# Performance work log

Measured on AMD Instinct MI355X. Metric: run time of the kernel, lower is better.

## Reference

```python
import jax, jax.numpy as jnp
import numpy as np

LN_EPS = 1e-6

def _layernorm(x, g, b):
    mu = jnp.mean(x, axis=-1, keepdims=True)
    var = jnp.mean((x - mu) ** 2, axis=-1, keepdims=True)
    return (x - mu) / jnp.sqrt(var + LN_EPS) * g + b

def _mha(q, k, v, wq, bq, wk, bk, wv, bv, fc, fcb, ln_g, ln_b, n_head, d_k, d_v):
    # standard post-LN multi-head attention (residual + layernorm), eval mode (no dropout)
    b, lq, _ = q.shape
    bk_, lk, _ = k.shape
    residual = q
    qh = (q @ wq + bq).reshape(b, lq, n_head, d_k).transpose(0, 2, 1, 3)      # [b,h,lq,dk]
    kh = (k @ wk + bk).reshape(bk_, lk, n_head, d_k).transpose(0, 2, 1, 3)    # [bk,h,lk,dk]
    vh = (v @ wv + bv).reshape(bk_, lk, n_head, d_v).transpose(0, 2, 1, 3)    # [bk,h,lk,dv]
    attn = jax.nn.softmax(jnp.matmul(qh, kh.swapaxes(-1, -2)) / (d_k ** 0.5), axis=-1)  # [b,h,lq,lk]
    out = jnp.matmul(attn, vh)                                                # [b,h,lq,dv]
    out = out.transpose(0, 2, 1, 3).reshape(b, lq, n_head * d_v)
    pre = out
    out = _layernorm(out @ fc + fcb + residual, ln_g, ln_b)
    return out, attn, pre


def setup_inputs() -> dict:
    key = jax.random.key(0)
    ks = jax.random.split(key, 32)
    B, C, H, W = 16, 64, 32, 32
    NC, D = 5, 96  # num_classes, memory feature dim
    s = 0.05
    d = {
        'x': jax.random.normal(ks[0], (B, C, H, W), jnp.float32),
        'memory': jax.random.normal(ks[1], (NC, D), jnp.float32),
        'wb_w': jax.random.normal(ks[2], (C, NC), jnp.float32) * s,
        'wb_b': jnp.zeros((NC,), jnp.float32),
        # slf_attn: n_head=1, d_model=64, d_input_k=96, d_k=96, d_v=64
        'a1_wq': jax.random.normal(ks[3], (64, 96), jnp.float32) * s,
        'a1_bq': jnp.zeros((96,), jnp.float32),
        'a1_wk': jax.random.normal(ks[4], (96, 96), jnp.float32) * s,
        'a1_bk': jnp.zeros((96,), jnp.float32),
        'a1_wv': jax.random.normal(ks[5], (96, 64), jnp.float32) * s,
        'a1_bv': jnp.zeros((64,), jnp.float32),
        'a1_fc': jax.random.normal(ks[6], (64, 64), jnp.float32) * s,
        'a1_fcb': jnp.zeros((64,), jnp.float32),
        'a1_ln_g': jnp.ones((64,), jnp.float32),
        'a1_ln_b': jnp.zeros((64,), jnp.float32),
        # slf_attn1: n_head=4, d_model=64, d_input_k=64, d_k=64, d_v=64
        'a2_wq': jax.random.normal(ks[7], (64, 256), jnp.float32) * s,
        'a2_bq': jnp.zeros((256,), jnp.float32),
        'a2_wk': jax.random.normal(ks[8], (64, 256), jnp.float32) * s,
        'a2_bk': jnp.zeros((256,), jnp.float32),
        'a2_wv': jax.random.normal(ks[9], (64, 256), jnp.float32) * s,
        'a2_bv': jnp.zeros((256,), jnp.float32),
        'a2_fc': jax.random.normal(ks[10], (256, 64), jnp.float32) * s,
        'a2_fcb': jnp.zeros((64,), jnp.float32),
        'a2_ln_g': jnp.ones((64,), jnp.float32),
        'a2_ln_b': jnp.zeros((64,), jnp.float32),
    }
    return d


def reference(x, memory, wb_w, wb_b,
              a1_wq, a1_bq, a1_wk, a1_bk, a1_wv, a1_bv, a1_fc, a1_fcb, a1_ln_g, a1_ln_b,
              a2_wq, a2_bq, a2_wk, a2_bk, a2_wv, a2_bv, a2_fc, a2_fcb, a2_ln_g, a2_ln_b):
    b, c, H, W = x.shape
    xt = x.transpose(0, 2, 3, 1).reshape(b, H * W, c)            # [b,HW,64]
    weight = xt @ wb_w + wb_b                                    # [b,HW,5]
    weight1 = jax.nn.softmax(weight, axis=-1)                    # softmax over classes
    weight2 = jax.nn.softmax(weight.transpose(0, 2, 1), axis=-1) # [b,5,HW], softmax over HW
    class_feat1 = jnp.matmul(weight2, xt)                        # [b,5,64] class-weighted pooling
    mem = memory[None]                                           # [1,5,96]
    cf, _, _ = _mha(class_feat1, mem, mem,
                    a1_wq, a1_bq, a1_wk, a1_bk, a1_wv, a1_bv, a1_fc, a1_fcb, a1_ln_g, a1_ln_b,
                    n_head=1, d_k=96, d_v=64)                    # [b,5,64]
    cf = jnp.matmul(weight1, cf)                                 # redistribution [b,HW,64]
    cf, _, _ = _mha(cf, cf, cf,
                    a2_wq, a2_bq, a2_wk, a2_bk, a2_wv, a2_bv, a2_fc, a2_fcb, a2_ln_g, a2_ln_b,
                    n_head=4, d_k=64, d_v=64)                    # [b,HW,64]
    return cf.transpose(0, 2, 1).reshape(-1, 64, H, W)           # [b,64,H,W]
```

## Files before the change

kernel.cpp:

```cpp
#include <hip/hip_runtime.h>
#include <math.h>

typedef unsigned short ushort_t;
typedef __attribute__((ext_vector_type(8))) short short8;
typedef __attribute__((ext_vector_type(4))) float f32x4;

#define B_  16
#define HW_ 1024
#define C_  64
#define NC_ 5
#define D1_ 96
#define NH_ 4
#define DH_ 64

#define MFMA32(A,B,C) __builtin_amdgcn_mfma_f32_16x16x32_bf16(A,B,C,0,0,0)

__device__ __forceinline__ ushort_t f2bf(float f) {
    unsigned u = __float_as_uint(f);
    u = u + 0x7fffu + ((u >> 16) & 1u);
    return (ushort_t)(u >> 16);
}

__device__ __forceinline__ unsigned pack2_trunc(float lo, float hi) {
    return (__float_as_uint(hi) & 0xffff0000u) | (__float_as_uint(lo) >> 16);
}
__device__ __forceinline__ unsigned pack2_rne(float lo, float hi) {
    return ((unsigned)f2bf(hi) << 16) | (unsigned)f2bf(lo);
}
__device__ __forceinline__ float bf_lo(unsigned u) { return __uint_as_float(u << 16); }
__device__ __forceinline__ float bf_hi(unsigned u) { return __uint_as_float(u & 0xffff0000u); }

__global__ __launch_bounds__(64) void k1_logits(const float* __restrict__ x,
                                                const float* __restrict__ wb_w,
                                                const float* __restrict__ wb_b,
                                                float* __restrict__ logitsT,
                                                float* __restrict__ w1) {
    int b = blockIdx.x >> 4;
    int hw = (blockIdx.x & 15) * 64 + threadIdx.x;
    const float* xb = x + (size_t)b * C_ * HW_;
    float acc[NC_];
#pragma unroll
    for (int j = 0; j < NC_; j++) acc[j] = wb_b[j];
#pragma unroll 8
    for (int c = 0; c < C_; c++) {
        float xv = xb[c * HW_ + hw];
#pragma unroll
        for (int j = 0; j < NC_; j++) acc[j] += xv * wb_w[c * NC_ + j];
    }
    float m = acc[0];
#pragma unroll
    for (int j = 1; j < NC_; j++) m = fmaxf(m, acc[j]);
    float e[NC_], s = 0.f;
#pragma unroll
    for (int j = 0; j < NC_; j++) { e[j] = __expf(acc[j] - m); s += e[j]; }
    float inv = 1.f / s;
    int idx = b * HW_ + hw;
#pragma unroll
    for (int j = 0; j < NC_; j++) {
        logitsT[((size_t)b * NC_ + j) * HW_ + hw] = acc[j];
        w1[(size_t)idx * NC_ + j] = e[j] * inv;
    }
}

__global__ __launch_bounds__(256) void k2b_pool(const float* __restrict__ x,
                                                const float* __restrict__ logitsT,
                                                float* __restrict__ cf1) {
    __shared__ float pl[NC_ * HW_];
    __shared__ float sinv[NC_];
    int t = threadIdx.x;
    int b = blockIdx.x >> 4, chg = blockIdx.x & 15;
    const float* lp = logitsT + (size_t)b * NC_ * HW_;
    for (int i = t * 4; i < NC_ * HW_; i += 1024)
        *(float4*)(pl + i) = *(const float4*)(lp + i);
    __syncthreads();
    int w = t >> 6, lane = t & 63;
    for (int r = w; r < NC_; r += 4) {
        float m = -1e30f;
        for (int i = lane; i < HW_; i += 64) m = fmaxf(m, pl[r * HW_ + i]);
#pragma unroll
        for (int off = 1; off < 64; off <<= 1) m = fmaxf(m, __shfl_xor(m, off, 64));
        float s = 0.f;
        for (int i = lane; i < HW_; i += 64) {
            float e = __expf(pl[r * HW_ + i] - m);
            pl[r * HW_ + i] = e;
            s += e;
        }
#pragma unroll
        for (int off = 1; off < 64; off <<= 1) s += __shfl_xor(s, off, 64);
        if (lane == 0) sinv[r] = 1.f / s;
    }
    __syncthreads();
    int ch = chg * 4 + w;
    const float* xc = x + ((size_t)b * C_ + ch) * HW_;
    float acc[NC_] = {0.f, 0.f, 0.f, 0.f, 0.f};
#pragma unroll
    for (int i = 0; i < HW_ / 64; i++) {
        int hw = i * 64 + lane;
        float xv = xc[hw];
#pragma unroll
        for (int c = 0; c < NC_; c++) acc[c] += xv * pl[c * HW_ + hw];
    }
#pragma unroll
    for (int c = 0; c < NC_; c++) {
        float a = acc[c];
#pragma unroll
        for (int off = 1; off < 64; off <<= 1) a += __shfl_xor(a, off, 64);
        if (lane == 0) cf1[((size_t)b * NC_ + c) * C_ + ch] = a * sinv[c];
    }
}

__global__ __launch_bounds__(256) void k3_mha1(const float* __restrict__ cf1,
                                               const float* __restrict__ wq, const float* __restrict__ bq,
                                               const float* __restrict__ mem,
                                               const float* __restrict__ wk, const float* __restrict__ bk,
                                               const float* __restrict__ wv, const float* __restrict__ bv,
                                               const float* __restrict__ fc, const float* __restrict__ fcb,
                                               const float* __restrict__ lng, const float* __restrict__ lnb,
                                               float* __restrict__ cfs) {
    __shared__ float cs[NC_ * C_];
    __shared__ float kh[NC_ * D1_];
    __shared__ float vh[NC_ * DH_];
    __shared__ float q[NC_ * D1_];
    __shared__ float sc[NC_ * NC_];
    __shared__ float pp[NC_ * NC_];
    __shared__ float o[NC_ * C_];
    __shared__ float z[NC_ * C_];
    __shared__ float mu[NC_], rs[NC_];
    int t = threadIdx.x, b = blockIdx.x;
    for (int i = t; i < NC_ * C_; i += 256) cs[i] = cf1[(size_t)b * NC_ * C_ + i];
    for (int idx = t; idx < NC_ * D1_; idx += 256) {
        int i = idx / D1_, k = idx % D1_;
        float a = bk[k];
        for (int d = 0; d < D1_; d++) a += mem[i * D1_ + d] * wk[d * D1_ + k];
        kh[idx] = a;
    }
    for (int idx = t; idx < NC_ * DH_; idx += 256) {
        int i = idx / DH_, dv = idx % DH_;
        float a = bv[dv];
        for (int d = 0; d < D1_; d++) a += mem[i * D1_ + d] * wv[d * DH_ + dv];
        vh[idx] = a;
    }
    __syncthreads();
    for (int idx = t; idx < NC_ * D1_; idx += 256) {
        int i = idx / D1_, k = idx % D1_;
        float a = bq[k];
        for (int c = 0; c < C_; c++) a += cs[i * C_ + c] * wq[c * D1_ + k];
        q[idx] = a;
    }
    __syncthreads();
    if (t < NC_ * NC_) {
        int i = t / NC_, j = t % NC_;
        float a = 0.f;
        for (int k = 0; k < D1_; k++) a += q[i * D1_ + k] * kh[j * D1_ + k];
        sc[t] = a * 0.1020620726159657f;
    }
    __syncthreads();
    if (t < NC_) {
        float m = sc[t * NC_];
        for (int j = 1; j < NC_; j++) m = fmaxf(m, sc[t * NC_ + j]);
        float e[NC_], s = 0.f;
        for (int j = 0; j < NC_; j++) { e[j] = __expf(sc[t * NC_ + j] - m); s += e[j]; }
        float inv = 1.f / s;
        for (int j = 0; j < NC_; j++) pp[t * NC_ + j] = e[j] * inv;
    }
    __syncthreads();
    for (int idx = t; idx < NC_ * C_; idx += 256) {
        int i = idx / C_, dv = idx % C_;
        float a = 0.f;
        for (int j = 0; j < NC_; j++) a += pp[i * NC_ + j] * vh[j * C_ + dv];
        o[idx] = a;
    }
    __syncthreads();
    for (int idx = t; idx < NC_ * C_; idx += 256) {
        int i = idx / C_, dd = idx % C_;
        float a = fcb[dd] + cs[idx];
        for (int c2 = 0; c2 < C_; c2++) a += o[i * C_ + c2] * fc[c2 * C_ + dd];
        z[idx] = a;
    }
    __syncthreads();
    if (t < NC_) {
        float s = 0.f;
        for (int d = 0; d < C_; d++) s += z[t * C_ + d];
        float mm = s / C_;
        float v = 0.f;
        for (int d = 0; d < C_; d++) { float dd2 = z[t * C_ + d] - mm; v += dd2 * dd2; }
        mu[t] = mm; rs[t] = rsqrtf(v / C_ + 1e-6f);
    }
    __syncthreads();
    for (int idx = t; idx < NC_ * C_; idx += 256) {
        int i = idx / C_, dd = idx % C_;
        cfs[(size_t)b * NC_ * C_ + idx] = (z[idx] - mu[i]) * rs[i] * lng[dd] + lnb[dd];
    }
}

__global__ __launch_bounds__(256) void k5_mfma(const float* __restrict__ w1,
                                               const float* __restrict__ cfs,
                                               const float* __restrict__ wq, const float* __restrict__ bq,
                                               const float* __restrict__ wk, const float* __restrict__ bk,
                                               const float* __restrict__ wv, const float* __restrict__ bv,
                                               ushort_t* __restrict__ Qb, ushort_t* __restrict__ Kb,
                                               ushort_t* __restrict__ Vt) {
    __shared__ ushort_t Af[64][68];
    __shared__ ushort_t Wt[256][68];
    int t = threadIdx.x;
    int which = blockIdx.y;
    int m0 = blockIdx.x * 64;
    int b = m0 >> 10, lbase = m0 & 1023;
    {
        int r = t >> 2, ks = (t & 3) * 16;
        const float* cp = cfs + (size_t)b * NC_ * C_;
        const float* w1p = w1 + (size_t)(m0 + r) * NC_;
        float v0 = w1p[0], v1 = w1p[1], v2 = w1p[2], v3 = w1p[3], v4 = w1p[4];
#pragma unroll
        for (int j = 0; j < 16; j += 2) {
            int k = ks + j;
            float e0 = v0 * cp[k]       + v1 * cp[64 + k]     + v2 * cp[128 + k]
                     + v3 * cp[192 + k] + v4 * cp[256 + k];
            float e1 = v0 * cp[k + 1]     + v1 * cp[64 + k + 1] + v2 * cp[128 + k + 1]
                     + v3 * cp[192 + k + 1] + v4 * cp[256 + k + 1];
            *(unsigned*)&Af[r][k] = pack2_rne(e0, e1);
        }
    }
    const float* W = (which == 0) ? wq : (which == 1) ? wk : wv;
    {
        int n = t;
#pragma unroll
        for (int k = 0; k < 64; k += 2) {
            *(unsigned*)&Wt[n][k] = pack2_rne(W[k * 256 + n], W[(k + 1) * 256 + n]);
        }
    }
    __syncthreads();
    int lane = t & 63, w = t >> 6;
    int l15 = lane & 15, quad = lane >> 4;
    if (which < 2) {
        const float* bias = (which == 0) ? bq : bk;
        float scale = (which == 0) ? 0.18033688011112042f : 1.0f;
        ushort_t* dst = (which == 0) ? Qb : Kb;
        short8 a0[4], a1[4];
#pragma unroll
        for (int mi = 0; mi < 4; mi++) {
            a0[mi] = *(const short8*)&Af[mi * 16 + l15][quad * 8];
            a1[mi] = *(const short8*)&Af[mi * 16 + l15][32 + quad * 8];
        }
#pragma unroll
        for (int nt = 0; nt < 4; nt++) {
            int ni = w * 4 + nt;
            short8 b0 = *(const short8*)&Wt[ni * 16 + l15][quad * 8];
            short8 b1 = *(const short8*)&Wt[ni * 16 + l15][32 + quad * 8];
            int n = ni * 16 + l15;
            float bb = bias[n];
            int h = n >> 6, dd = n & 63;
#pragma unroll
            for (int mi = 0; mi < 4; mi++) {
                f32x4 z = {0, 0, 0, 0};
                f32x4 dv4 = MFMA32(a0[mi], b0, z);
                dv4 = MFMA32(a1[mi], b1, dv4);
                size_t base = ((size_t)(b * NH_ + h) * HW_ + (lbase + mi * 16 + quad * 4)) * DH_ + dd;
#pragma unroll
                for (int r = 0; r < 4; r++)
                    dst[base + (size_t)r * DH_] = f2bf((dv4[r] + bb) * scale);
            }
        }
    } else {
        short8 a0[4], a1[4];
#pragma unroll
        for (int mt = 0; mt < 4; mt++) {
            int mi = w * 4 + mt;
            a0[mt] = *(const short8*)&Wt[mi * 16 + l15][quad * 8];
            a1[mt] = *(const short8*)&Wt[mi * 16 + l15][32 + quad * 8];
        }
#pragma unroll
        for (int nt = 0; nt < 4; nt++) {
            short8 b0 = *(const short8*)&Af[nt * 16 + l15][quad * 8];
            short8 b1 = *(const short8*)&Af[nt * 16 + l15][32 + quad * 8];
#pragma unroll
            for (int mt = 0; mt < 4; mt++) {
                int mi = w * 4 + mt;
                f32x4 z = {0, 0, 0, 0};
                f32x4 dv4 = MFMA32(a0[mt], b0, z);
                dv4 = MFMA32(a1[mt], b1, dv4);
                int h = mi >> 2;
#pragma unroll
                for (int r = 0; r < 4; r++) {
                    int nw = mi * 16 + quad * 4 + r;
                    int dv = nw & 63;
                    Vt[((size_t)(b * NH_ + h) * DH_ + dv) * HW_ + lbase + nt * 16 + l15] =
                        f2bf(dv4[r] + bv[nw]);
                }
            }
        }
    }
}

__global__ __launch_bounds__(256) void k6_attn(const ushort_t* __restrict__ Qb,
                                               const ushort_t* __restrict__ Kb,
                                               const ushort_t* __restrict__ Vt,
                                               ushort_t* __restrict__ aoP0, ushort_t* __restrict__ aoP1,
                                               float* __restrict__ sP0, float* __restrict__ sP1) {
    int t = threadIdx.x;
    int w = t >> 6;
    int lane = t & 63;
    int l15 = lane & 15;
    int quad = lane >> 4;
    int L = blockIdx.x;
    int bh = ((L >> 3) & 7) * 8 + (L & 7);
    int khalf = (L >> 6) & 1;
    int qt = L >> 7;
    int b = bh >> 2, h = bh & 3;
    const ushort_t* Qp = Qb + (size_t)bh * HW_ * DH_;
    const ushort_t* Kp = Kb + (size_t)bh * HW_ * DH_;
    const ushort_t* Vp = Vt + (size_t)bh * DH_ * HW_;
    int row0 = qt * 256 + w * 16;
    short8 q0[4], q1[4];
#pragma unroll
    for (int tl = 0; tl < 4; tl++) {
        const ushort_t* qp = Qp + (size_t)(row0 + tl * 64 + l15) * DH_ + quad * 8;
        q0[tl] = *(const short8*)(qp);
        q1[tl] = *(const short8*)(qp + 32);
    }
    int f0 = ((l15 >> 2) * 8) + (l15 & 3);
    int kstart = khalf * 512;
    const ushort_t* K0p = Kp + (size_t)(kstart + f0) * DH_ + quad * 8;
    const ushort_t* K1p = Kp + (size_t)(kstart + f0 + 4) * DH_ + quad * 8;
    const ushort_t* Vp0 = Vp + (size_t)(0 * 16 + l15) * HW_ + kstart + quad * 8;
    const ushort_t* Vp1 = Vp + (size_t)(1 * 16 + l15) * HW_ + kstart + quad * 8;
    const ushort_t* Vp2 = Vp + (size_t)(2 * 16 + l15) * HW_ + kstart + quad * 8;
    const ushort_t* Vp3 = Vp + (size_t)(3 * 16 + l15) * HW_ + kstart + quad * 8;
    const short ONE = (short)0x3F80;
    short8 ones = {ONE, ONE, ONE, ONE, ONE, ONE, ONE, ONE};
    f32x4 o0[4], o1[4], o2[4], o3[4], oS[4];
#pragma unroll
    for (int tl = 0; tl < 4; tl++) {
        o0[tl] = (f32x4){0,0,0,0}; o1[tl] = (f32x4){0,0,0,0};
        o2[tl] = (f32x4){0,0,0,0}; o3[tl] = (f32x4){0,0,0,0};
        oS[tl] = (f32x4){0,0,0,0};
    }
    for (int kt = 0; kt < 16; kt++) {
        int kbase = kt * 32;
        size_t koff = (size_t)kbase * DH_;
        short8 ka0 = *(const short8*)(K0p + koff);
        short8 ka1 = *(const short8*)(K0p + koff + 32);
        short8 kb0 = *(const short8*)(K1p + koff);
        short8 kb1 = *(const short8*)(K1p + koff + 32);
        short8 v0 = *(const short8*)(Vp0 + kbase);
        short8 v1 = *(const short8*)(Vp1 + kbase);
        short8 v2 = *(const short8*)(Vp2 + kbase);
        short8 v3 = *(const short8*)(Vp3 + kbase);
        f32x4 z = {0,0,0,0};
#pragma unroll
        for (int tl = 0; tl < 4; tl++) {
            f32x4 s0 = MFMA32(ka0, q0[tl], z);  s0 = MFMA32(ka1, q1[tl], s0);
            f32x4 s1 = MFMA32(kb0, q0[tl], z);  s1 = MFMA32(kb1, q1[tl], s1);
            float p0 = exp2f(s0[0]), p1 = exp2f(s0[1]), p2 = exp2f(s0[2]), p3 = exp2f(s0[3]);
            float p4 = exp2f(s1[0]), p5 = exp2f(s1[1]), p6 = exp2f(s1[2]), p7 = exp2f(s1[3]);
            union { short8 v; unsigned u[4]; } pf;
            pf.u[0] = pack2_trunc(p0, p1);  pf.u[1] = pack2_trunc(p2, p3);
            pf.u[2] = pack2_trunc(p4, p5);  pf.u[3] = pack2_trunc(p6, p7);
            o0[tl] = MFMA32(v0, pf.v, o0[tl]);
            o1[tl] = MFMA32(v1, pf.v, o1[tl]);
            o2[tl] = MFMA32(v2, pf.v, o2[tl]);
            o3[tl] = MFMA32(v3, pf.v, o3[tl]);
            oS[tl] = MFMA32(ones, pf.v, oS[tl]);
        }
    }
    ushort_t* aoP = khalf ? aoP1 : aoP0;
    float* sP = khalf ? sP1 : sP0;
#pragma unroll
    for (int tl = 0; tl < 4; tl++) {
        int rowg = row0 + tl * 64 + l15;
        ushort_t* aop = aoP + ((size_t)(b * HW_ + rowg)) * 256 + h * 64 + quad * 4;
        uint2 u;
        u.x = pack2_trunc(o0[tl][0], o0[tl][1]); u.y = pack2_trunc(o0[tl][2], o0[tl][3]);
        *(uint2*)(aop + 0) = u;
        u.x = pack2_trunc(o1[tl][0], o1[tl][1]); u.y = pack2_trunc(o1[tl][2], o1[tl][3]);
        *(uint2*)(aop + 16) = u;
        u.x = pack2_trunc(o2[tl][0], o2[tl][1]); u.y = pack2_trunc(o2[tl][2], o2[tl][3]);
        *(uint2*)(aop + 32) = u;
        u.x = pack2_trunc(o3[tl][0], o3[tl][1]); u.y = pack2_trunc(o3[tl][2], o3[tl][3]);
        *(uint2*)(aop + 48) = u;
        if (quad == 0)
            sP[(size_t)(b * HW_ + rowg) * NH_ + h] = oS[tl][0];
    }
}

__global__ __launch_bounds__(256) void k7_final(const ushort_t* __restrict__ aoP0,
                                                const ushort_t* __restrict__ aoP1,
                                                const float* __restrict__ sP0,
                                                const float* __restrict__ sP1,
                                                const float* __restrict__ w1,
                                                const float* __restrict__ cfs,
                                                const float* __restrict__ fc, const float* __restrict__ fcb,
                                                const float* __restrict__ lng, const float* __restrict__ lnb,
                                                float* __restrict__ out) {
    __shared__ float srow[16 * 256];
    __shared__ float rinv[64];
    __shared__ float T[64 * 17];
    int t = threadIdx.x, w = t >> 6, d = t & 63;
    int m0 = blockIdx.x * 16;
    int b = m0 >> 10;
    if (t < 64) {
        int row = t >> 2, hh = t & 3;
        float s = sP0[(size_t)(m0 + row) * NH_ + hh] + sP1[(size_t)(m0 + row) * NH_ + hh];
        rinv[t] = 1.f / s;
    }
    __syncthreads();
    for (int i = t; i < 512; i += 256) {
        uint4 a  = *(const uint4*)(aoP0 + (size_t)m0 * 256 + i * 8);
        uint4 c4 = *(const uint4*)(aoP1 + (size_t)m0 * 256 + i * 8);
        int e = i * 8, row = e >> 8, hh = (e >> 6) & 3;
        float r = rinv[row * 4 + hh];
        srow[e + 0] = (bf_lo(a.x) + bf_lo(c4.x)) * r;
        srow[e + 1] = (bf_hi(a.x) + bf_hi(c4.x)) * r;
        srow[e + 2] = (bf_lo(a.y) + bf_lo(c4.y)) * r;
        srow[e + 3] = (bf_hi(a.y) + bf_hi(c4.y)) * r;
        srow[e + 4] = (bf_lo(a.z) + bf_lo(c4.z)) * r;
        srow[e + 5] = (bf_hi(a.z) + bf_hi(c4.z)) * r;
        srow[e + 6] = (bf_lo(a.w) + bf_lo(c4.w)) * r;
        srow[e + 7] = (bf_hi(a.w) + bf_hi(c4.w)) * r;
    }
    __syncthreads();
    float bias = fcb[d];
    const float* cp = cfs + (size_t)b * NC_ * C_;
    float a[4];
#pragma unroll
    for (int j = 0; j < 4; j++) {
        int m = m0 + w * 4 + j;
        const float* w1p = w1 + (size_t)m * NC_;
        float acc = bias;
#pragma unroll
        for (int c = 0; c < NC_; c++) acc += w1p[c] * cp[c * 64 + d];
        a[j] = acc;
    }
#pragma unroll 4
    for (int k4 = 0; k4 < 64; k4++) {
        int k = k4 * 4;
        float f0 = fc[(k + 0) * 64 + d];
        float f1 = fc[(k + 1) * 64 + d];
        float f2 = fc[(k + 2) * 64 + d];
        float f3 = fc[(k + 3) * 64 + d];
#pragma unroll
        for (int j = 0; j < 4; j++) {
            float4 s = *(const float4*)&srow[(w * 4 + j) * 256 + k];
            a[j] += s.x * f0 + s.y * f1 + s.z * f2 + s.w * f3;
        }
    }
    float g = lng[d], be = lnb[d];
#pragma unroll
    for (int j = 0; j < 4; j++) {
        float s1 = a[j], s2 = a[j] * a[j];
#pragma unroll
        for (int off = 1; off < 64; off <<= 1) {
            s1 += __shfl_xor(s1, off, 64);
            s2 += __shfl_xor(s2, off, 64);
        }
        float mu = s1 * (1.f / 64.f);
        float var = s2 * (1.f / 64.f) - mu * mu;
        float rstd = rsqrtf(var + 1e-6f);
        T[d * 17 + w * 4 + j] = (a[j] - mu) * rstd * g + be;
    }
    __syncthreads();
    int ch = t >> 2, part = t & 3;
    int hw0 = m0 & 1023;
    float4 v = {T[ch * 17 + part * 4 + 0], T[ch * 17 + part * 4 + 1],
                T[ch * 17 + part * 4 + 2], T[ch * 17 + part * 4 + 3]};
    *(float4*)&out[((size_t)b * 64 + ch) * 1024 + hw0 + part * 4] = v;
}

extern "C" void kernel_launch(void* const* d_in, const int* in_sizes, int n_in,
                              void* d_out, int out_size, void* d_ws, size_t ws_size,
                              hipStream_t stream) {
    const float* x      = (const float*)d_in[0];
    const float* memory = (const float*)d_in[1];
    const float* wb_w   = (const float*)d_in[2];
    const float* wb_b   = (const float*)d_in[3];
    const float* a1_wq  = (const float*)d_in[4];
    const float* a1_bq  = (const float*)d_in[5];
    const float* a1_wk  = (const float*)d_in[6];
    const float* a1_bk  = (const float*)d_in[7];
    const float* a1_wv  = (const float*)d_in[8];
    const float* a1_bv  = (const float*)d_in[9];
    const float* a1_fc  = (const float*)d_in[10];
    const float* a1_fcb = (const float*)d_in[11];
    const float* a1_ln_g = (const float*)d_in[12];
    const float* a1_ln_b = (const float*)d_in[13];
    const float* a2_wq  = (const float*)d_in[14];
    const float* a2_bq  = (const float*)d_in[15];
    const float* a2_wk  = (const float*)d_in[16];
    const float* a2_bk  = (const float*)d_in[17];
    const float* a2_wv  = (const float*)d_in[18];
    const float* a2_bv  = (const float*)d_in[19];
    const float* a2_fc  = (const float*)d_in[20];
    const float* a2_fcb = (const float*)d_in[21];
    const float* a2_ln_g = (const float*)d_in[22];
    const float* a2_ln_b = (const float*)d_in[23];

    float* ws = (float*)d_ws;
    float* logitsT = ws;
    float* w1  = logitsT + 81920;
    float* cf1 = w1 + 81920;
    float* cfs = cf1 + 5120;
    float* sP0 = cfs + 5120;
    float* sP1 = sP0 + 65536;
    ushort_t* aoP0 = (ushort_t*)(sP1 + 65536);
    ushort_t* aoP1 = aoP0 + 4194304;
    ushort_t* Qb = aoP1 + 4194304;
    ushort_t* Kb = Qb + 4194304;
    ushort_t* Vt = Kb + 4194304;

    k1_logits<<<256, 64, 0, stream>>>(x, wb_w, wb_b, logitsT, w1);
    k2b_pool<<<256, 256, 0, stream>>>(x, logitsT, cf1);
    k3_mha1<<<16, 256, 0, stream>>>(cf1, a1_wq, a1_bq, memory, a1_wk, a1_bk,
                                    a1_wv, a1_bv, a1_fc, a1_fcb,
                                    a1_ln_g, a1_ln_b, cfs);
    k5_mfma<<<dim3(256, 3), 256, 0, stream>>>(w1, cfs, a2_wq, a2_bq, a2_wk, a2_bk,
                                              a2_wv, a2_bv, Qb, Kb, Vt);
    k6_attn<<<512, 256, 0, stream>>>(Qb, Kb, Vt, aoP0, aoP1, sP0, sP1);
    k7_final<<<1024, 256, 0, stream>>>(aoP0, aoP1, sP0, sP1, w1, cfs, a2_fc, a2_fcb,
                                       a2_ln_g, a2_ln_b, (float*)d_out);
}
```

Before: 202.5 us.

## Double-buffer K/V tiles in LDS for attention and use MFMA for output projection

In the attention kernel, the per-iteration K and V fragment loads from global memory are replaced by a double-buffered LDS staging scheme using global_load_lds. Each wave loads one slice for the next tile while the current tile is being computed. This is meant to hide global memory latency and stop every wave from fetching the same K/V data redundantly. The final kernel now runs the 256->64 fc projection with bf16 MFMA against a pre-packed bf16 weight layout written by a new small kernel, replacing the scalar FP32 loop. The cost is an extra launch, a barrier per tile, and lower precision in the fc projection.

```diff
diff --git a/kernel.cpp b/kernel.cpp
--- a/kernel.cpp
+++ b/kernel.cpp
@@ -29,6 +29,25 @@
 }
 __device__ __forceinline__ float bf_lo(unsigned u) { return __uint_as_float(u << 16); }
 __device__ __forceinline__ float bf_hi(unsigned u) { return __uint_as_float(u & 0xffff0000u); }
+
+__device__ __forceinline__ void gload16(const ushort_t* g, ushort_t* l) {
+    __builtin_amdgcn_global_load_lds(
+        (const __attribute__((address_space(1))) unsigned int*)g,
+        (__attribute__((address_space(3))) unsigned int*)l,
+        16, 0, 0);
+}
+
+__global__ __launch_bounds__(256) void k0_fcT(const float* __restrict__ fc,
+                                              ushort_t* __restrict__ F) {
+    int c = blockIdx.x * 256 + threadIdx.x;
+    int l = c & 63, s = (c >> 6) & 7, n = c >> 9;
+    int col = n * 16 + (l & 15);
+    int k0 = s * 32 + (l >> 4) * 8;
+    union { ushort_t us[8]; uint4 u; } pk;
+#pragma unroll
+    for (int j = 0; j < 8; j++) pk.us[j] = f2bf(fc[(k0 + j) * 64 + col]);
+    *(uint4*)(F + (size_t)c * 8) = pk.u;
+}
 
 __global__ __launch_bounds__(64) void k1_logits(const float* __restrict__ x,
                                                 const float* __restrict__ wb_w,
@@ -297,6 +316,7 @@
                                                const ushort_t* __restrict__ Vt,
                                                ushort_t* __restrict__ aoP0, ushort_t* __restrict__ aoP1,
                                                float* __restrict__ sP0, float* __restrict__ sP1) {
+    __shared__ ushort_t Kst[2][8][512];
     int t = threadIdx.x;
     int w = t >> 6;
     int lane = t & 63;
@@ -326,6 +346,23 @@
     const ushort_t* Vp1 = Vp + (size_t)(1 * 16 + l15) * HW_ + kstart + quad * 8;
     const ushort_t* Vp2 = Vp + (size_t)(2 * 16 + l15) * HW_ + kstart + quad * 8;
     const ushort_t* Vp3 = Vp + (size_t)(3 * 16 + l15) * HW_ + kstart + quad * 8;
+    auto stage = [&](int kt, int bb) {
+        size_t koff = (size_t)kt * 32 * DH_;
+        int kb32 = kt * 32;
+        if (w == 0) {
+            gload16(K0p + koff,      &Kst[bb][0][0]);
+            gload16(K0p + koff + 32, &Kst[bb][1][0]);
+        } else if (w == 1) {
+            gload16(K1p + koff,      &Kst[bb][2][0]);
+            gload16(K1p + koff + 32, &Kst[bb][3][0]);
+        } else if (w == 2) {
+            gload16(Vp0 + kb32, &Kst[bb][4][0]);
+            gload16(Vp1 + kb32, &Kst[bb][5][0]);
+        } else {
+            gload16(Vp2 + kb32, &Kst[bb][6][0]);
+            gload16(Vp3 + kb32, &Kst[bb][7][0]);
+        }
+    };
     const short ONE = (short)0x3F80;
     short8 ones = {ONE, ONE, ONE, ONE, ONE, ONE, ONE, ONE};
     f32x4 o0[4], o1[4], o2[4], o3[4], oS[4];
@@ -335,17 +372,20 @@
         o2[tl] = (f32x4){0,0,0,0}; o3[tl] = (f32x4){0,0,0,0};
         oS[tl] = (f32x4){0,0,0,0};
     }
+    stage(0, 0);
     for (int kt = 0; kt < 16; kt++) {
-        int kbase = kt * 32;
-        size_t koff = (size_t)kbase * DH_;
-        short8 ka0 = *(const short8*)(K0p + koff);
-        short8 ka1 = *(const short8*)(K0p + koff + 32);
-        short8 kb0 = *(const short8*)(K1p + koff);
-        short8 kb1 = *(const short8*)(K1p + koff + 32);
-        short8 v0 = *(const short8*)(Vp0 + kbase);
-        short8 v1 = *(const short8*)(Vp1 + kbase);
-        short8 v2 = *(const short8*)(Vp2 + kbase);
-        short8 v3 = *(const short8*)(Vp3 + kbase);
+        int bb = kt & 1;
+        __syncthreads();
+        if (kt < 15) stage(kt + 1, bb ^ 1);
+        const ushort_t* S = &Kst[bb][0][0];
+        short8 ka0 = *(const short8*)(S + 0 * 512 + lane * 8);
+        short8 ka1 = *(const short8*)(S + 1 * 512 + lane * 8);
+        short8 kb0 = *(const short8*)(S + 2 * 512 + lane * 8);
+        short8 kb1 = *(const short8*)(S + 3 * 512 + lane * 8);
+        short8 v0  = *(const short8*)(S + 4 * 512 + lane * 8);
+        short8 v1  = *(const short8*)(S + 5 * 512 + lane * 8);
+        short8 v2  = *(const short8*)(S + 6 * 512 + lane * 8);
+        short8 v3  = *(const short8*)(S + 7 * 512 + lane * 8);
         f32x4 z = {0,0,0,0};
 #pragma unroll
         for (int tl = 0; tl < 4; tl++) {
@@ -389,65 +429,63 @@
                                                 const float* __restrict__ sP1,
                                                 const float* __restrict__ w1,
                                                 const float* __restrict__ cfs,
-                                                const float* __restrict__ fc, const float* __restrict__ fcb,
+                                                const ushort_t* __restrict__ F,
+                                                const float* __restrict__ fcb,
                                                 const float* __restrict__ lng, const float* __restrict__ lnb,
                                                 float* __restrict__ out) {
-    __shared__ float srow[16 * 256];
+    __shared__ ushort_t Afr[512 * 8];
     __shared__ float rinv[64];
-    __shared__ float T[64 * 17];
-    int t = threadIdx.x, w = t >> 6, d = t & 63;
-    int m0 = blockIdx.x * 16;
-    int b = m0 >> 10;
+    __shared__ float T[16][68];
+    __shared__ float To[64 * 17];
+    int t = threadIdx.x, w = t >> 6, lane = t & 63;
+    int m0 = blockIdx.x * 16, b = m0 >> 10;
     if (t < 64) {
         int row = t >> 2, hh = t & 3;
         float s = sP0[(size_t)(m0 + row) * NH_ + hh] + sP1[(size_t)(m0 + row) * NH_ + hh];
         rinv[t] = 1.f / s;
     }
     __syncthreads();
-    for (int i = t; i < 512; i += 256) {
-        uint4 a  = *(const uint4*)(aoP0 + (size_t)m0 * 256 + i * 8);
-        uint4 c4 = *(const uint4*)(aoP1 + (size_t)m0 * 256 + i * 8);
-        int e = i * 8, row = e >> 8, hh = (e >> 6) & 3;
+#pragma unroll
+    for (int cc = t; cc < 512; cc += 256) {
+        int s = cc >> 6, l = cc & 63;
+        int row = l & 15, col0 = s * 32 + (l >> 4) * 8;
+        int hh = col0 >> 6;
+        size_t base = (size_t)(m0 + row) * 256 + col0;
+        uint4 a = *(const uint4*)(aoP0 + base);
+        uint4 c4 = *(const uint4*)(aoP1 + base);
         float r = rinv[row * 4 + hh];
-        srow[e + 0] = (bf_lo(a.x) + bf_lo(c4.x)) * r;
-        srow[e + 1] = (bf_hi(a.x) + bf_hi(c4.x)) * r;
-        srow[e + 2] = (bf_lo(a.y) + bf_lo(c4.y)) * r;
-        srow[e + 3] = (bf_hi(a.y) + bf_hi(c4.y)) * r;
-        srow[e + 4] = (bf_lo(a.z) + bf_lo(c4.z)) * r;
-        srow[e + 5] = (bf_hi(a.z) + bf_hi(c4.z)) * r;
-        srow[e + 6] = (bf_lo(a.w) + bf_lo(c4.w)) * r;
-        srow[e + 7] = (bf_hi(a.w) + bf_hi(c4.w)) * r;
-    }
-    __syncthreads();
-    float bias = fcb[d];
+        uint4 pk;
+        pk.x = pack2_trunc((bf_lo(a.x) + bf_lo(c4.x)) * r, (bf_hi(a.x) + bf_hi(c4.x)) * r);
+        pk.y = pack2_trunc((bf_lo(a.y) + bf_lo(c4.y)) * r, (bf_hi(a.y) + bf_hi(c4.y)) * r);
+        pk.z = pack2_trunc((bf_lo(a.z) + bf_lo(c4.z)) * r, (bf_hi(a.z) + bf_hi(c4.z)) * r);
+        pk.w = pack2_trunc((bf_lo(a.w) + bf_lo(c4.w)) * r, (bf_hi(a.w) + bf_hi(c4.w)) * r);
+        *(uint4*)&Afr[(size_t)cc * 8] = pk;
+    }
+    __syncthreads();
+    f32x4 acc = {0, 0, 0, 0};
+#pragma unroll
+    for (int s = 0; s < 8; s++) {
+        short8 a = *(const short8*)&Afr[(s * 64 + lane) * 8];
+        short8 bf8 = *(const short8*)(F + ((size_t)(w * 8 + s) * 64 + lane) * 8);
+        acc = MFMA32(a, bf8, acc);
+    }
+    {
+        int l15 = lane & 15, quad = lane >> 4;
+#pragma unroll
+        for (int r = 0; r < 4; r++) T[quad * 4 + r][w * 16 + l15] = acc[r];
+    }
+    __syncthreads();
+    int d = lane;
+    float g = lng[d], be = lnb[d], bias = fcb[d];
     const float* cp = cfs + (size_t)b * NC_ * C_;
-    float a[4];
 #pragma unroll
     for (int j = 0; j < 4; j++) {
-        int m = m0 + w * 4 + j;
-        const float* w1p = w1 + (size_t)m * NC_;
-        float acc = bias;
-#pragma unroll
-        for (int c = 0; c < NC_; c++) acc += w1p[c] * cp[c * 64 + d];
-        a[j] = acc;
-    }
-#pragma unroll 4
-    for (int k4 = 0; k4 < 64; k4++) {
-        int k = k4 * 4;
-        float f0 = fc[(k + 0) * 64 + d];
-        float f1 = fc[(k + 1) * 64 + d];
-        float f2 = fc[(k + 2) * 64 + d];
-        float f3 = fc[(k + 3) * 64 + d];
-#pragma unroll
-        for (int j = 0; j < 4; j++) {
-            float4 s = *(const float4*)&srow[(w * 4 + j) * 256 + k];
-            a[j] += s.x * f0 + s.y * f1 + s.z * f2 + s.w * f3;
-        }
-    }
-    float g = lng[d], be = lnb[d];
-#pragma unroll
-    for (int j = 0; j < 4; j++) {
-        float s1 = a[j], s2 = a[j] * a[j];
+        int row = w * 4 + j;
+        const float* w1p = w1 + (size_t)(m0 + row) * NC_;
+        float a = bias + T[row][d];
+#pragma unroll
+        for (int c = 0; c < NC_; c++) a += w1p[c] * cp[c * 64 + d];
+        float s1 = a, s2 = a * a;
 #pragma unroll
         for (int off = 1; off < 64; off <<= 1) {
             s1 += __shfl_xor(s1, off, 64);
@@ -456,13 +494,13 @@
         float mu = s1 * (1.f / 64.f);
         float var = s2 * (1.f / 64.f) - mu * mu;
         float rstd = rsqrtf(var + 1e-6f);
-        T[d * 17 + w * 4 + j] = (a[j] - mu) * rstd * g + be;
+        To[d * 17 + row] = (a - mu) * rstd * g + be;
     }
     __syncthreads();
     int ch = t >> 2, part = t & 3;
     int hw0 = m0 & 1023;
-    float4 v = {T[ch * 17 + part * 4 + 0], T[ch * 17 + part * 4 + 1],
-                T[ch * 17 + part * 4 + 2], T[ch * 17 + part * 4 + 3]};
+    float4 v = {To[ch * 17 + part * 4 + 0], To[ch * 17 + part * 4 + 1],
+                To[ch * 17 + part * 4 + 2], To[ch * 17 + part * 4 + 3]};
     *(float4*)&out[((size_t)b * 64 + ch) * 1024 + hw0 + part * 4] = v;
 }
 
@@ -506,7 +544,9 @@
     ushort_t* Qb = aoP1 + 4194304;
     ushort_t* Kb = Qb + 4194304;
     ushort_t* Vt = Kb + 4194304;
-
+    ushort_t* F  = Vt + 4194304;
+
+    k0_fcT<<<8, 256, 0, stream>>>(a2_fc, F);
     k1_logits<<<256, 64, 0, stream>>>(x, wb_w, wb_b, logitsT, w1);
     k2b_pool<<<256, 256, 0, stream>>>(x, logitsT, cf1);
     k3_mha1<<<16, 256, 0, stream>>>(cf1, a1_wq, a1_bq, memory, a1_wk, a1_bk,
@@ -515,6 +555,6 @@
     k5_mfma<<<dim3(256, 3), 256, 0, stream>>>(w1, cfs, a2_wq, a2_bq, a2_wk, a2_bk,
                                               a2_wv, a2_bv, Qb, Kb, Vt);
     k6_attn<<<512, 256, 0, stream>>>(Qb, Kb, Vt, aoP0, aoP1, sP0, sP1);
-    k7_final<<<1024, 256, 0, stream>>>(aoP0, aoP1, sP0, sP1, w1, cfs, a2_fc, a2_fcb,
+    k7_final<<<1024, 256, 0, stream>>>(aoP0, aoP1, sP0, sP1, w1, cfs, F, a2_fcb,
                                        a2_ln_g, a2_ln_b, (float*)d_out);
 }
```

Result: faster. 191.5 us (-5.5%).
